# Kernel optimization log

Hardware: AMD Instinct MI355X
Metric: run time of the kernel (lower is better)

## Reference

```python
import jax, jax.numpy as jnp
import numpy as np

B, F, P, DM = 1, 16, 256, 1024            # batch, frames, patches, mm_hidden_size
HID = 4096                                 # config.hidden_size
DI, DSTATE, DTRANK, DCONV = 2 * DM, 16, DM // 16, 4


def _layernorm(x, w, b):
    mu = x.mean(-1, keepdims=True)
    var = ((x - mu) ** 2).mean(-1, keepdims=True)
    return (x - mu) * jax.lax.rsqrt(var + 1e-5) * w + b


def _selective_scan(u, dt, A, Bm, Cm, Dv):
    # u, dt: [b,L,d]; Bm, Cm: [b,L,n]; A: [d,n]; Dv: [d]
    def step(h, inp):
        dt_t, B_t, C_t, u_t = inp  # [b,d],[b,n],[b,n],[b,d]
        h = jnp.exp(dt_t[..., None] * A) * h + (dt_t * u_t)[..., None] * B_t[:, None, :]
        return h, jnp.einsum('bdn,bn->bd', h, C_t)
    h0 = jnp.zeros((u.shape[0], A.shape[0], A.shape[1]), u.dtype)
    _, ys = jax.lax.scan(step, h0, (jnp.swapaxes(dt, 0, 1), jnp.swapaxes(Bm, 0, 1),
                                    jnp.swapaxes(Cm, 0, 1), jnp.swapaxes(u, 0, 1)))
    return jnp.swapaxes(ys, 0, 1) + u * Dv


def _mamba_block(x, ln_w, ln_b, in_proj_w, conv_w, conv_b, x_proj_w,
                 dt_proj_w, dt_proj_b, A_log, D_param, out_proj_w):
    res = x
    x = _layernorm(x, ln_w, ln_b)
    xz = x @ in_proj_w                       # [b,L,2*DI]
    xin, z = jnp.split(xz, 2, axis=-1)
    xt = jnp.swapaxes(xin, 1, 2)             # [b,DI,L]
    xt = jax.lax.conv_general_dilated(xt, conv_w[:, None, :], (1,), [(DCONV - 1, 0)],
                                      dimension_numbers=('NCH', 'OIH', 'NCH'),
                                      feature_group_count=DI)
    xt = xt + conv_b[:, None]
    u = jax.nn.silu(jnp.swapaxes(xt, 1, 2))  # [b,L,DI]
    x_dbl = u @ x_proj_w                     # [b,L,DTRANK+2*DSTATE]
    dt_raw, Bm, Cm = jnp.split(x_dbl, [DTRANK, DTRANK + DSTATE], axis=-1)
    dt = jax.nn.softplus(dt_raw @ dt_proj_w + dt_proj_b)
    A = -jnp.exp(A_log)
    y = _selective_scan(u, dt, A, Bm, Cm, D_param)
    y = y * jax.nn.silu(z)
    return res + y @ out_proj_w


def setup_inputs() -> dict:
    key = jax.random.key(0)
    ks = jax.random.split(key, 8)
    s = 0.02
    return {
        'vst': jax.random.normal(ks[0], (B, F, P, DM), jnp.float32),
        'ln_w': jnp.ones((DM,), jnp.float32), 'ln_b': jnp.zeros((DM,), jnp.float32),
        'in_proj_w': jax.random.normal(ks[1], (DM, 2 * DI), jnp.float32) * s,
        'conv_w': jax.random.normal(ks[2], (DI, DCONV), jnp.float32) * s,
        'conv_b': jnp.zeros((DI,), jnp.float32),
        'x_proj_w': jax.random.normal(ks[3], (DI, DTRANK + 2 * DSTATE), jnp.float32) * s,
        'dt_proj_w': jax.random.normal(ks[4], (DTRANK, DI), jnp.float32) * s,
        'dt_proj_b': jnp.full((DI,), -4.6, jnp.float32),  # softplus ~ 0.01
        'A_log': jnp.log(jnp.tile(jnp.arange(1, DSTATE + 1, dtype=jnp.float32), (DI, 1))),
        'D_param': jnp.ones((DI,), jnp.float32),
        'out_proj_w': jax.random.normal(ks[5], (DI, DM), jnp.float32) * s,
        'fln_w': jnp.ones((DM,), jnp.float32), 'fln_b': jnp.zeros((DM,), jnp.float32),
        'mlp_w1': jax.random.normal(ks[6], (DM, HID), jnp.float32) * s,
        'mlp_b1': jnp.zeros((HID,), jnp.float32),
        'mlp_w2': jax.random.normal(ks[7], (HID, HID), jnp.float32) * s,
        'mlp_b2': jnp.zeros((HID,), jnp.float32),
    }


def reference(vst, ln_w, ln_b, in_proj_w, conv_w, conv_b, x_proj_w, dt_proj_w,
              dt_proj_b, A_log, D_param, out_proj_w, fln_w, fln_b,
              mlp_w1, mlp_b1, mlp_w2, mlp_b2):
    b, f, p, d = vst.shape
    h = w = int(p ** 0.5)
    # the chain of rearranges in the source is a net reshape to b (f h w) d
    x = vst.reshape(b, f * h * w, d)
    x = _mamba_block(x, ln_w, ln_b, in_proj_w, conv_w, conv_b, x_proj_w,
                     dt_proj_w, dt_proj_b, A_log, D_param, out_proj_w)
    x = _layernorm(x, fln_w, fln_b)
    # AvgPool3d kernel=(1,4,4), stride=(1,4,4) over (f,h,w)
    x = x.reshape(b, f, h // 4, 4, w // 4, 4, d).mean(axis=(3, 5))
    x = x.reshape(b, f * (h // 4) * (w // 4), d)
    y = jax.nn.gelu(x @ mlp_w1 + mlp_b1, approximate=False)
    return y @ mlp_w2 + mlp_b2
```

## Files before the change

kernel.cpp:

```cpp
#include <hip/hip_runtime.h>
#include <hip/hip_bf16.h>
#include <math.h>

typedef __hip_bfloat16 bf16_t;
typedef __attribute__((ext_vector_type(8))) short short8;
typedef __attribute__((ext_vector_type(4))) float f32x4;

#define L_SEQ   4096
#define DMODEL  1024
#define DI      2048
#define NST     16
#define DTRANK  64
#define XDBL_N  96
#define HID     4096
#define CHUNK   32
#define NCHUNK  128
#define POOLED_ROWS 256

__device__ __forceinline__ void async_load16(const bf16_t* g, bf16_t* l) {
    __builtin_amdgcn_global_load_lds(
        (const __attribute__((address_space(1))) void*)g,
        (__attribute__((address_space(3))) void*)l,
        16, 0, 0);
}

__device__ __forceinline__ float bfbits2f(unsigned short b) {
    bf16_t h; *(unsigned short*)&h = b; return __bfloat162float(h);
}

__global__ __launch_bounds__(256)
void transpose_all_kernel(const float* __restrict__ j0, bf16_t* __restrict__ o0,
                          const float* __restrict__ j1, bf16_t* __restrict__ o1,
                          const float* __restrict__ j2, bf16_t* __restrict__ o2,
                          const float* __restrict__ j3, bf16_t* __restrict__ o3,
                          const float* __restrict__ j4, bf16_t* __restrict__ o4,
                          const float* __restrict__ j5, bf16_t* __restrict__ o5) {
    int b = blockIdx.x;
    const float* in; bf16_t* out; int K, N, Npad, local;
    if (b < 512)        { in = j0; out = o0; K = 1024; N = 4096; Npad = 4096; local = b; }
    else if (b < 544)   { in = j1; out = o1; K = 2048; N = 96;   Npad = 128;  local = b - 512; }
    else if (b < 576)   { in = j2; out = o2; K = 64;   N = 2048; Npad = 2048; local = b - 544; }
    else if (b < 832)   { in = j3; out = o3; K = 2048; N = 1024; Npad = 1024; local = b - 576; }
    else if (b < 1344)  { in = j4; out = o4; K = 1024; N = 4096; Npad = 4096; local = b - 832; }
    else                { in = j5; out = o5; K = 4096; N = 4096; Npad = 4096; local = b - 1344; }
    int nt = Npad >> 6;
    int k0 = (local / nt) << 7, n0 = (local % nt) << 6;

    __shared__ float t[64 * 129];
    int tid = threadIdx.x;
    int kkb = tid >> 4;
    int nq  = (tid & 15) * 4;
#pragma unroll
    for (int it = 0; it < 8; it++) {
        int kl = it * 16 + kkb;
        int gk = k0 + kl, gn = n0 + nq;
        float4 v = {0.f, 0.f, 0.f, 0.f};
        if (gk < K) {
            const float* src = in + (size_t)gk * N + gn;
            if (gn + 3 < N) v = *(const float4*)src;
            else {
                if (gn + 0 < N) v.x = src[0];
                if (gn + 1 < N) v.y = src[1];
                if (gn + 2 < N) v.z = src[2];
                if (gn + 3 < N) v.w = src[3];
            }
        }
        t[(nq + 0) * 129 + kl] = v.x;
        t[(nq + 1) * 129 + kl] = v.y;
        t[(nq + 2) * 129 + kl] = v.z;
        t[(nq + 3) * 129 + kl] = v.w;
    }
    __syncthreads();
#pragma unroll
    for (int it = 0; it < 4; it++) {
        int slot = it * 256 + tid;
        int nn = slot >> 4, kc = (slot & 15) * 8;
        if (k0 + kc >= K) continue;
        const float* r = &t[nn * 129 + kc];
        short8 o;
#pragma unroll
        for (int j = 0; j < 8; j++) {
            bf16_t h = __float2bfloat16(r[j]);
            o[j] = *(short*)&h;
        }
        *(short8*)(out + (size_t)(n0 + nn) * K + k0 + kc) = o;
    }
}

__global__ __launch_bounds__(256)
void ln_kernel(const float* __restrict__ x, const float* __restrict__ w,
               const float* __restrict__ b, bf16_t* __restrict__ out) {
    int row = blockIdx.x;
    int tid = threadIdx.x;
    const float* xr = x + (size_t)row * DMODEL;
    float v[4];
    float s = 0.f, ss = 0.f;
#pragma unroll
    for (int e = 0; e < 4; e++) {
        v[e] = xr[tid + e * 256];
        s += v[e];
        ss += v[e] * v[e];
    }
#pragma unroll
    for (int off = 32; off > 0; off >>= 1) {
        s  += __shfl_down(s, off);
        ss += __shfl_down(ss, off);
    }
    __shared__ float rs[4], rss[4];
    int wid = tid >> 6;
    if ((tid & 63) == 0) { rs[wid] = s; rss[wid] = ss; }
    __syncthreads();
    s  = rs[0] + rs[1] + rs[2] + rs[3];
    ss = rss[0] + rss[1] + rss[2] + rss[3];
    float mu  = s * (1.f / DMODEL);
    float var = ss * (1.f / DMODEL) - mu * mu;
    float inv = rsqrtf(var + 1e-5f);
#pragma unroll
    for (int e = 0; e < 4; e++) {
        int col = tid + e * 256;
        out[(size_t)row * DMODEL + col] =
            __float2bfloat16((v[e] - mu) * inv * w[col] + b[col]);
    }
}

__global__ __launch_bounds__(256)
void ln_pool2_kernel(const bf16_t* __restrict__ part, size_t pstride,
                     const float* __restrict__ res, const float* __restrict__ w,
                     const float* __restrict__ b, bf16_t* __restrict__ pooled) {
    int p = blockIdx.x;
    int tid = threadIdx.x;
    int f = p >> 4, i4 = (p >> 2) & 3, j4 = p & 3;
    __shared__ float rs[4], rss[4];
    float acc[4] = {0.f, 0.f, 0.f, 0.f};
    float wv[4], bv[4];
#pragma unroll
    for (int e = 0; e < 4; e++) { wv[e] = w[tid + e * 256]; bv[e] = b[tid + e * 256]; }
    for (int r16 = 0; r16 < 16; r16++) {
        int ii = r16 >> 2, jj = r16 & 3;
        int row = f * 256 + (i4 * 4 + ii) * 16 + j4 * 4 + jj;
        size_t ro = (size_t)row * DMODEL;
        float v[4];
        float s = 0.f, ss = 0.f;
#pragma unroll
        for (int e = 0; e < 4; e++) {
            int col = tid + e * 256;
            float x = res[ro + col]
                    + __bfloat162float(part[ro + col])
                    + __bfloat162float(part[pstride + ro + col]);
            v[e] = x;
            s += x;
            ss += x * x;
        }
#pragma unroll
        for (int off = 32; off > 0; off >>= 1) {
            s  += __shfl_down(s, off);
            ss += __shfl_down(ss, off);
        }
        int wid = tid >> 6;
        if ((tid & 63) == 0) { rs[wid] = s; rss[wid] = ss; }
        __syncthreads();
        s  = rs[0] + rs[1] + rs[2] + rs[3];
        ss = rss[0] + rss[1] + rss[2] + rss[3];
        float mu  = s * (1.f / DMODEL);
        float var = ss * (1.f / DMODEL) - mu * mu;
        float inv = rsqrtf(var + 1e-5f);
#pragma unroll
        for (int e = 0; e < 4; e++)
            acc[e] += (v[e] - mu) * inv * wv[e] + bv[e];
        __syncthreads();
    }
#pragma unroll
    for (int e = 0; e < 4; e++)
        pooled[(size_t)p * DMODEL + tid + e * 256] = __float2bfloat16(acc[e] * (1.f / 16.f));
}

template <int EPI>
__global__ __launch_bounds__(256, 2)
void mfma_gemm(const bf16_t* __restrict__ A, int lda,
               const bf16_t* __restrict__ Bt, int ldb,
               int K,
               float* __restrict__ Cf, bf16_t* __restrict__ Cb, int ldc,
               const float* __restrict__ bias, const float* __restrict__ res) {
    __shared__ bf16_t Asl[128 * 32];
    __shared__ bf16_t Bsl[128 * 32];
    const int tid = threadIdx.x;
    const int l = tid & 63, w = tid >> 6;
    const int m0 = blockIdx.y * 128, n0 = blockIdx.x * 128;
    const int wm = (w >> 1) * 64, wn = (w & 1) * 64;

    const int srow = tid >> 2;
    const int skc = (tid & 3) * 8;
    const bf16_t* Ag = A + (size_t)(m0 + srow) * lda + skc;
    const bf16_t* Bg = Bt + (size_t)(n0 + srow) * ldb + skc;
    bf16_t* As0 = Asl + (size_t)(w * 64) * 8;
    bf16_t* As1 = Asl + (size_t)(256 + w * 64) * 8;
    bf16_t* Bs0 = Bsl + (size_t)(w * 64) * 8;
    bf16_t* Bs1 = Bsl + (size_t)(256 + w * 64) * 8;

    f32x4 acc[4][4];
#pragma unroll
    for (int i = 0; i < 4; i++)
#pragma unroll
        for (int j = 0; j < 4; j++) acc[i][j] = (f32x4){0.f, 0.f, 0.f, 0.f};

    const short8* Asv = (const short8*)Asl;
    const short8* Bsv = (const short8*)Bsl;
    const int fr = l >> 4;
    const int fc = l & 15;

    for (int k0 = 0; k0 < K; k0 += 32) {
        __syncthreads();
        async_load16(Ag, As0);
        async_load16(Ag + (size_t)64 * lda, As1);
        async_load16(Bg, Bs0);
        async_load16(Bg + (size_t)64 * ldb, Bs1);
        Ag += 32; Bg += 32;
        __syncthreads();

        short8 a[4], b[4];
#pragma unroll
        for (int im = 0; im < 4; im++)
            a[im] = Asv[(wm + im * 16 + fc) * 4 + fr];
#pragma unroll
        for (int in = 0; in < 4; in++)
            b[in] = Bsv[(wn + in * 16 + fc) * 4 + fr];
#pragma unroll
        for (int im = 0; im < 4; im++)
#pragma unroll
            for (int in = 0; in < 4; in++)
                acc[im][in] = __builtin_amdgcn_mfma_f32_16x16x32_bf16(
                    a[im], b[in], acc[im][in], 0, 0, 0);
    }

#pragma unroll
    for (int im = 0; im < 4; im++) {
        int mbase = m0 + wm + im * 16 + fr * 4;
#pragma unroll
        for (int in = 0; in < 4; in++) {
            int n = n0 + wn + in * 16 + fc;
            float bv = (EPI == 1) ? bias[n] : 0.f;
#pragma unroll
            for (int v = 0; v < 4; v++) {
                float x = acc[im][in][v];
                size_t off = (size_t)(mbase + v) * ldc + n;
                if (EPI == 0) {
                    Cb[off] = __float2bfloat16(x);
                } else if (EPI == 1) {
                    x += bv;
                    x = (x > 20.f) ? x : log1pf(__expf(x));
                    Cb[off] = __float2bfloat16(x);
                }
            }
        }
    }
}

template <bool PBF16>
__global__ __launch_bounds__(256, 2)
void mfma_gemm_splitk(const bf16_t* __restrict__ A, int lda,
                      const bf16_t* __restrict__ Bt, int ldb,
                      int Kper, void* __restrict__ Cpart, int ldc,
                      size_t pstride) {
    __shared__ bf16_t Asl[128 * 32];
    __shared__ bf16_t Bsl[128 * 32];
    const int tid = threadIdx.x;
    const int l = tid & 63, w = tid >> 6;
    const int m0 = blockIdx.y * 128, n0 = blockIdx.x * 128;
    const int wm = (w >> 1) * 64, wn = (w & 1) * 64;
    const int kbase = blockIdx.z * Kper;

    const int srow = tid >> 2;
    const int skc = (tid & 3) * 8;
    const bf16_t* Ag = A + (size_t)(m0 + srow) * lda + kbase + skc;
    const bf16_t* Bg = Bt + (size_t)(n0 + srow) * ldb + kbase + skc;
    bf16_t* As0 = Asl + (size_t)(w * 64) * 8;
    bf16_t* As1 = Asl + (size_t)(256 + w * 64) * 8;
    bf16_t* Bs0 = Bsl + (size_t)(w * 64) * 8;
    bf16_t* Bs1 = Bsl + (size_t)(256 + w * 64) * 8;

    f32x4 acc[4][4];
#pragma unroll
    for (int i = 0; i < 4; i++)
#pragma unroll
        for (int j = 0; j < 4; j++) acc[i][j] = (f32x4){0.f, 0.f, 0.f, 0.f};

    const short8* Asv = (const short8*)Asl;
    const short8* Bsv = (const short8*)Bsl;
    const int fr = l >> 4;
    const int fc = l & 15;

    for (int k0 = 0; k0 < Kper; k0 += 32) {
        __syncthreads();
        async_load16(Ag, As0);
        async_load16(Ag + (size_t)64 * lda, As1);
        async_load16(Bg, Bs0);
        async_load16(Bg + (size_t)64 * ldb, Bs1);
        Ag += 32; Bg += 32;
        __syncthreads();

        short8 a[4], b[4];
#pragma unroll
        for (int im = 0; im < 4; im++)
            a[im] = Asv[(wm + im * 16 + fc) * 4 + fr];
#pragma unroll
        for (int in = 0; in < 4; in++)
            b[in] = Bsv[(wn + in * 16 + fc) * 4 + fr];
#pragma unroll
        for (int im = 0; im < 4; im++)
#pragma unroll
            for (int in = 0; in < 4; in++)
                acc[im][in] = __builtin_amdgcn_mfma_f32_16x16x32_bf16(
                    a[im], b[in], acc[im][in], 0, 0, 0);
    }

#pragma unroll
    for (int im = 0; im < 4; im++) {
        int mbase = m0 + wm + im * 16 + fr * 4;
#pragma unroll
        for (int in = 0; in < 4; in++) {
            int n = n0 + wn + in * 16 + fc;
#pragma unroll
            for (int v = 0; v < 4; v++) {
                size_t o = (size_t)(mbase + v) * ldc + n;
                if (PBF16)
                    ((bf16_t*)Cpart)[(size_t)blockIdx.z * pstride + o] =
                        __float2bfloat16(acc[im][in][v]);
                else
                    ((float*)Cpart)[(size_t)blockIdx.z * pstride + o] = acc[im][in][v];
            }
        }
    }
}

template <int S, int EPI>
__global__ __launch_bounds__(256)
void reduce_splitk(const float* __restrict__ part, size_t pstride, int ldp,
                   int M, int N, float* __restrict__ outf, bf16_t* __restrict__ outb,
                   int ldo, const float* __restrict__ bias) {
    int idx = blockIdx.x * 256 + threadIdx.x;
    if (idx >= M * N) return;
    int r = idx / N, c = idx - r * N;
    float s = 0.f;
#pragma unroll
    for (int z = 0; z < S; z++)
        s += part[(size_t)z * pstride + (size_t)r * ldp + c];
    size_t o = (size_t)r * ldo + c;
    if (EPI == 0) {
        outf[o] = s;
        outb[o] = __float2bfloat16(s);
    } else if (EPI == 1) {
        s += bias[c];
        s = 0.5f * s * (1.f + erff(s * 0.70710678118654752f));
        outb[o] = __float2bfloat16(s);
    } else {
        outf[o] = s + bias[c];
    }
}

__global__ __launch_bounds__(256)
void conv_silu_kernel(const bf16_t* __restrict__ xz, const float* __restrict__ cw,
                      const float* __restrict__ cb, bf16_t* __restrict__ u) {
    int idx = blockIdx.x * 256 + threadIdx.x;
    if (idx >= L_SEQ * DI) return;
    int ch = idx & (DI - 1);
    int l  = idx >> 11;
    float acc = cb[ch];
#pragma unroll
    for (int k = 0; k < 4; k++) {
        int ls = l - 3 + k;
        if (ls >= 0)
            acc += cw[ch * 4 + k] * __bfloat162float(xz[(size_t)ls * (2 * DI) + ch]);
    }
    u[idx] = __float2bfloat16(acc / (1.f + __expf(-acc)));
}

__global__ __launch_bounds__(256)
void scan_pass1(const bf16_t* __restrict__ dt, const bf16_t* __restrict__ u,
                const float* __restrict__ x_dbl, const float* __restrict__ A_log,
                float* __restrict__ Pw, float* __restrict__ Sw) {
    int c = blockIdx.x;
    int tid = threadIdx.x;
    int lane = tid & 63, w = tid >> 6;
    int dloc = w * 32 + (lane & 31);
    int n0 = (lane >> 5) * 8;
    int d = blockIdx.y * 128 + dloc;
    int l0 = c * CHUNK;
    __shared__ float sB[CHUNK * NST];
    for (int i = tid; i < CHUNK * NST; i += 256)
        sB[i] = x_dbl[(size_t)(l0 + (i >> 4)) * XDBL_N + DTRANK + (i & 15)];
    __syncthreads();
    float Areg[8], h[8];
#pragma unroll
    for (int j = 0; j < 8; j++) {
        Areg[j] = -__expf(A_log[d * NST + n0 + j]);
        h[j] = 0.f;
    }
    float dts = 0.f;
    float dtl = __bfloat162float(dt[(size_t)l0 * DI + d]);
    float ul  = __bfloat162float(u[(size_t)l0 * DI + d]);
    for (int l = 0; l < CHUNK; l++) {
        float dtn = 0.f, un = 0.f;
        if (l + 1 < CHUNK) {
            int gl = l0 + l + 1;
            dtn = __bfloat162float(dt[(size_t)gl * DI + d]);
            un  = __bfloat162float(u[(size_t)gl * DI + d]);
        }
        float du = dtl * ul;
        dts += dtl;
#pragma unroll
        for (int j = 0; j < 8; j++) {
            float a = __expf(dtl * Areg[j]);
            h[j] = a * h[j] + du * sB[l * NST + n0 + j];
        }
        dtl = dtn; ul = un;
    }
    size_t base = ((size_t)c * DI + d) * NST + n0;
#pragma unroll
    for (int j = 0; j < 8; j++) {
        Pw[base + j] = __expf(dts * Areg[j]);
        Sw[base + j] = h[j];
    }
}

__global__ __launch_bounds__(256)
void scan_pass2(const float* __restrict__ Pw, float* __restrict__ SwInit) {
    int tid = blockIdx.x * 256 + threadIdx.x;
    if (tid >= DI * NST) return;
    const int DN = DI * NST;
    size_t idx = tid;
    float h = 0.f;
    float p = Pw[idx], s = SwInit[idx];
    for (int c = 0; c < NCHUNK; c++) {
        size_t nidx = idx + DN;
        float pn = 0.f, sn = 0.f;
        if (c + 1 < NCHUNK) { pn = Pw[nidx]; sn = SwInit[nidx]; }
        SwInit[idx] = h;
        h = p * h + s;
        p = pn; s = sn; idx = nidx;
    }
}

__global__ __launch_bounds__(256)
void scan_pass3(const bf16_t* __restrict__ dt, const bf16_t* __restrict__ u,
                const float* __restrict__ x_dbl, const float* __restrict__ A_log,
                const float* __restrict__ Dp, const float* __restrict__ initw,
                const bf16_t* __restrict__ xz, bf16_t* __restrict__ yy) {
    int c = blockIdx.x;
    int tid = threadIdx.x;
    int lane = tid & 63, w = tid >> 6;
    int dloc = w * 32 + (lane & 31);
    int n0 = (lane >> 5) * 8;
    int d = blockIdx.y * 128 + dloc;
    int l0 = c * CHUNK;
    __shared__ float sBC[CHUNK * 2 * NST];
    for (int i = tid; i < CHUNK * 2 * NST; i += 256)
        sBC[i] = x_dbl[(size_t)(l0 + (i >> 5)) * XDBL_N + DTRANK + (i & 31)];
    __syncthreads();
    float Areg[8], h[8];
    size_t base = ((size_t)c * DI + d) * NST + n0;
#pragma unroll
    for (int j = 0; j < 8; j++) {
        Areg[j] = -__expf(A_log[d * NST + n0 + j]);
        h[j] = initw[base + j];
    }
    float Dd = Dp[d];
    float dtl = __bfloat162float(dt[(size_t)l0 * DI + d]);
    float ul  = __bfloat162float(u[(size_t)l0 * DI + d]);
    float zv  = __bfloat162float(xz[(size_t)l0 * (2 * DI) + DI + d]);
    for (int l = 0; l < CHUNK; l++) {
        float dtn = 0.f, un = 0.f, zn = 0.f;
        if (l + 1 < CHUNK) {
            int gl = l0 + l + 1;
            dtn = __bfloat162float(dt[(size_t)gl * DI + d]);
            un  = __bfloat162float(u[(size_t)gl * DI + d]);
            zn  = __bfloat162float(xz[(size_t)gl * (2 * DI) + DI + d]);
        }
        float du = dtl * ul;
        float y = 0.f;
#pragma unroll
        for (int j = 0; j < 8; j++) {
            float a = __expf(dtl * Areg[j]);
            h[j] = a * h[j] + du * sBC[l * 32 + n0 + j];
            y += h[j] * sBC[l * 32 + NST + n0 + j];
        }
        y += __shfl_xor(y, 32);
        float sz = zv / (1.f + __expf(-zv));
        if ((lane >> 5) == 0)
            yy[(size_t)(l0 + l) * DI + d] = __float2bfloat16((y + ul * Dd) * sz);
        dtl = dtn; ul = un; zv = zn;
    }
}

extern "C" void kernel_launch(void* const* d_in, const int* in_sizes, int n_in,
                              void* d_out, int out_size, void* d_ws, size_t ws_size,
                              hipStream_t stream) {
    const float* vst        = (const float*)d_in[0];
    const float* ln_w       = (const float*)d_in[1];
    const float* ln_b       = (const float*)d_in[2];
    const float* in_proj_w  = (const float*)d_in[3];
    const float* conv_w     = (const float*)d_in[4];
    const float* conv_b     = (const float*)d_in[5];
    const float* x_proj_w   = (const float*)d_in[6];
    const float* dt_proj_w  = (const float*)d_in[7];
    const float* dt_proj_b  = (const float*)d_in[8];
    const float* A_log      = (const float*)d_in[9];
    const float* D_param    = (const float*)d_in[10];
    const float* out_proj_w = (const float*)d_in[11];
    const float* fln_w      = (const float*)d_in[12];
    const float* fln_b      = (const float*)d_in[13];
    const float* mlp_w1     = (const float*)d_in[14];
    const float* mlp_b1     = (const float*)d_in[15];
    const float* mlp_w2     = (const float*)d_in[16];
    const float* mlp_b2     = (const float*)d_in[17];
    float* out = (float*)d_out;

    char* wsb = (char*)d_ws;
    size_t off = 0;
    auto alloc_bf = [&](size_t n) { bf16_t* p = (bf16_t*)(wsb + off); off += n * 2; return p; };
    auto alloc_f  = [&](size_t n) { float*  p = (float*)(wsb + off); off += n * 4; return p; };

    bf16_t* w1t  = alloc_bf((size_t)(2 * DI) * DMODEL);
    bf16_t* xpt  = alloc_bf((size_t)128 * DI);
    bf16_t* dtpt = alloc_bf((size_t)DI * DTRANK);
    bf16_t* opt  = alloc_bf((size_t)DMODEL * DI);
    bf16_t* m1t  = alloc_bf((size_t)HID * DMODEL);
    bf16_t* m2t  = alloc_bf((size_t)HID * HID);
    bf16_t* xz_bf   = alloc_bf((size_t)L_SEQ * 2 * DI);
    bf16_t* u_bf    = alloc_bf((size_t)L_SEQ * DI);
    bf16_t* dt_bf   = alloc_bf((size_t)L_SEQ * DI);
    bf16_t* xdbl_bf = alloc_bf((size_t)L_SEQ * XDBL_N);
    bf16_t* yy_bf   = alloc_bf((size_t)L_SEQ * DI);
    float*  xdbl_f  = alloc_f((size_t)L_SEQ * XDBL_N);
    float*  Pw      = alloc_f((size_t)NCHUNK * DI * NST);
    float*  Sw      = alloc_f((size_t)NCHUNK * DI * NST);
    bf16_t* xn_bf   = yy_bf;
    float*  g2part  = Pw;
    bf16_t* g4part  = xz_bf;
    bf16_t* pooled  = dt_bf;
    bf16_t* h1_bf   = dt_bf + (size_t)POOLED_ROWS * DMODEL;
    float*  g5part  = (float*)yy_bf;
    float*  g6part  = (float*)xz_bf;

    dim3 blk256(256);

    transpose_all_kernel<<<3392, blk256, 0, stream>>>(
        in_proj_w, w1t, x_proj_w, xpt, dt_proj_w, dtpt,
        out_proj_w, opt, mlp_w1, m1t, mlp_w2, m2t);

    ln_kernel<<<L_SEQ, blk256, 0, stream>>>(vst, ln_w, ln_b, xn_bf);

    mfma_gemm<0><<<dim3((2 * DI) / 128, L_SEQ / 128), blk256, 0, stream>>>(
        xn_bf, DMODEL, w1t, DMODEL, DMODEL, nullptr, xz_bf, 2 * DI, nullptr, nullptr);

    conv_silu_kernel<<<(L_SEQ * DI) / 256, blk256, 0, stream>>>(xz_bf, conv_w, conv_b, u_bf);

    mfma_gemm_splitk<false><<<dim3(1, L_SEQ / 128, 8), blk256, 0, stream>>>(
        u_bf, DI, xpt, DI, DI / 8, g2part, 128, (size_t)L_SEQ * 128);
    reduce_splitk<8, 0><<<(L_SEQ * XDBL_N) / 256, blk256, 0, stream>>>(
        g2part, (size_t)L_SEQ * 128, 128, L_SEQ, XDBL_N, xdbl_f, xdbl_bf, XDBL_N, nullptr);

    mfma_gemm<1><<<dim3(DI / 128, L_SEQ / 128), blk256, 0, stream>>>(
        xdbl_bf, XDBL_N, dtpt, DTRANK, DTRANK, nullptr, dt_bf, DI, dt_proj_b, nullptr);

    scan_pass1<<<dim3(NCHUNK, DI / 128), blk256, 0, stream>>>(
        dt_bf, u_bf, xdbl_f, A_log, Pw, Sw);
    scan_pass2<<<(DI * NST) / 256, blk256, 0, stream>>>(Pw, Sw);
    scan_pass3<<<dim3(NCHUNK, DI / 128), blk256, 0, stream>>>(
        dt_bf, u_bf, xdbl_f, A_log, D_param, Sw, xz_bf, yy_bf);

    mfma_gemm_splitk<true><<<dim3(DMODEL / 128, L_SEQ / 128, 2), blk256, 0, stream>>>(
        yy_bf, DI, opt, DI, DI / 2, g4part, DMODEL, (size_t)L_SEQ * DMODEL);

    ln_pool2_kernel<<<POOLED_ROWS, blk256, 0, stream>>>(
        g4part, (size_t)L_SEQ * DMODEL, vst, fln_w, fln_b, pooled);

    mfma_gemm_splitk<false><<<dim3(HID / 128, POOLED_ROWS / 128, 4), blk256, 0, stream>>>(
        pooled, DMODEL, m1t, DMODEL, DMODEL / 4, g5part, HID, (size_t)POOLED_ROWS * HID);
    reduce_splitk<4, 1><<<(POOLED_ROWS * HID) / 256, blk256, 0, stream>>>(
        g5part, (size_t)POOLED_ROWS * HID, HID, POOLED_ROWS, HID, nullptr, h1_bf, HID, mlp_b1);

    mfma_gemm_splitk<false><<<dim3(HID / 128, POOLED_ROWS / 128, 8), blk256, 0, stream>>>(
        h1_bf, HID, m2t, HID, HID / 8, g6part, HID, (size_t)POOLED_ROWS * HID);
    reduce_splitk<8, 2><<<(POOLED_ROWS * HID) / 256, blk256, 0, stream>>>(
        g6part, (size_t)POOLED_ROWS * HID, HID, POOLED_ROWS, HID, out, nullptr, HID, mlp_b2);
}
```

Baseline: 483.6 us.

## Consume fp32 mlp_w2 directly in a new split-K GEMM, skipping its transpose

Stops transposing and converting the 4096x4096 mlp_w2 matrix to bf16 in the preprocessing kernel. A new 512-thread split-K MFMA kernel loads the fp32 weight tiles into LDS asynchronously and converts them to bf16 while building the fragments. This removes a full read and write pass over the largest weight matrix. In exchange, the final GEMM reads fp32 weights, twice the bytes of bf16, and does per-element conversions in its inner loop.

```diff
diff --git a/kernel.cpp b/kernel.cpp
--- a/kernel.cpp
+++ b/kernel.cpp
@@ -17,32 +17,26 @@
 #define NCHUNK  128
 #define POOLED_ROWS 256
 
-__device__ __forceinline__ void async_load16(const bf16_t* g, bf16_t* l) {
+__device__ __forceinline__ void async_load16(const void* g, void* l) {
     __builtin_amdgcn_global_load_lds(
         (const __attribute__((address_space(1))) void*)g,
         (__attribute__((address_space(3))) void*)l,
         16, 0, 0);
 }
 
-__device__ __forceinline__ float bfbits2f(unsigned short b) {
-    bf16_t h; *(unsigned short*)&h = b; return __bfloat162float(h);
-}
-
 __global__ __launch_bounds__(256)
 void transpose_all_kernel(const float* __restrict__ j0, bf16_t* __restrict__ o0,
                           const float* __restrict__ j1, bf16_t* __restrict__ o1,
                           const float* __restrict__ j2, bf16_t* __restrict__ o2,
                           const float* __restrict__ j3, bf16_t* __restrict__ o3,
-                          const float* __restrict__ j4, bf16_t* __restrict__ o4,
-                          const float* __restrict__ j5, bf16_t* __restrict__ o5) {
+                          const float* __restrict__ j4, bf16_t* __restrict__ o4) {
     int b = blockIdx.x;
     const float* in; bf16_t* out; int K, N, Npad, local;
     if (b < 512)        { in = j0; out = o0; K = 1024; N = 4096; Npad = 4096; local = b; }
     else if (b < 544)   { in = j1; out = o1; K = 2048; N = 96;   Npad = 128;  local = b - 512; }
     else if (b < 576)   { in = j2; out = o2; K = 64;   N = 2048; Npad = 2048; local = b - 544; }
     else if (b < 832)   { in = j3; out = o3; K = 2048; N = 1024; Npad = 1024; local = b - 576; }
-    else if (b < 1344)  { in = j4; out = o4; K = 1024; N = 4096; Npad = 4096; local = b - 832; }
-    else                { in = j5; out = o5; K = 4096; N = 4096; Npad = 4096; local = b - 1344; }
+    else                { in = j4; out = o4; K = 1024; N = 4096; Npad = 4096; local = b - 832; }
     int nt = Npad >> 6;
     int k0 = (local / nt) << 7, n0 = (local % nt) << 6;
 
@@ -328,6 +322,81 @@
                 else
                     ((float*)Cpart)[(size_t)blockIdx.z * pstride + o] = acc[im][in][v];
             }
+        }
+    }
+}
+
+__global__ __launch_bounds__(512, 1)
+void gemm_nt_kernel(const bf16_t* __restrict__ A, int lda,
+                    const float* __restrict__ B, int ldb,
+                    int Kper, float* __restrict__ Cpart, int ldc,
+                    size_t pstride) {
+    __shared__ bf16_t Asl[256 * 32];
+    __shared__ float  Bsl[32 * 64];
+    const int tid = threadIdx.x;
+    const int l = tid & 63, w = tid >> 6;
+    const int n0 = blockIdx.x * 64;
+    const int kbase = blockIdx.z * Kper;
+    const int wm = w * 32;
+
+    const int a_row = tid >> 2, a_kc = (tid & 3) * 8;
+    const bf16_t* Ag = A + (size_t)a_row * lda + kbase + a_kc;
+    bf16_t* As0 = Asl + (size_t)(w * 64) * 8;
+    bf16_t* As1 = Asl + (size_t)(512 + w * 64) * 8;
+    const int b_row = tid >> 4, b_nc = (tid & 15) * 4;
+    const float* Bg = B + (size_t)(kbase + b_row) * ldb + n0 + b_nc;
+    float* Bs0 = Bsl + (size_t)(w * 64) * 4;
+
+    f32x4 acc[2][4];
+#pragma unroll
+    for (int i = 0; i < 2; i++)
+#pragma unroll
+        for (int j = 0; j < 4; j++) acc[i][j] = (f32x4){0.f, 0.f, 0.f, 0.f};
+
+    const short8* Asv = (const short8*)Asl;
+    const int fr = l >> 4, fc = l & 15;
+
+    for (int k0 = 0; k0 < Kper; k0 += 32) {
+        __syncthreads();
+        async_load16(Ag, As0);
+        async_load16(Ag + (size_t)128 * lda, As1);
+        async_load16(Bg, Bs0);
+        Ag += 32;
+        Bg += (size_t)32 * ldb;
+        __syncthreads();
+
+        short8 a[2], bfr[4];
+        a[0] = Asv[(wm + fc) * 4 + fr];
+        a[1] = Asv[(wm + 16 + fc) * 4 + fr];
+#pragma unroll
+        for (int j = 0; j < 4; j++) {
+            const float* bp = Bsl + (size_t)(fr * 8) * 64 + j * 16 + fc;
+            short8 t;
+#pragma unroll
+            for (int i = 0; i < 8; i++) {
+                bf16_t h = __float2bfloat16(bp[i * 64]);
+                t[i] = *(short*)&h;
+            }
+            bfr[j] = t;
+        }
+#pragma unroll
+        for (int im = 0; im < 2; im++)
+#pragma unroll
+            for (int j = 0; j < 4; j++)
+                acc[im][j] = __builtin_amdgcn_mfma_f32_16x16x32_bf16(
+                    a[im], bfr[j], acc[im][j], 0, 0, 0);
+    }
+
+    float* Cz = Cpart + (size_t)blockIdx.z * pstride;
+#pragma unroll
+    for (int im = 0; im < 2; im++) {
+        int mbase = wm + im * 16 + fr * 4;
+#pragma unroll
+        for (int j = 0; j < 4; j++) {
+            int n = n0 + j * 16 + fc;
+#pragma unroll
+            for (int v = 0; v < 4; v++)
+                Cz[(size_t)(mbase + v) * ldc + n] = acc[im][j][v];
         }
     }
 }
@@ -524,7 +593,6 @@
     bf16_t* dtpt = alloc_bf((size_t)DI * DTRANK);
     bf16_t* opt  = alloc_bf((size_t)DMODEL * DI);
     bf16_t* m1t  = alloc_bf((size_t)HID * DMODEL);
-    bf16_t* m2t  = alloc_bf((size_t)HID * HID);
     bf16_t* xz_bf   = alloc_bf((size_t)L_SEQ * 2 * DI);
     bf16_t* u_bf    = alloc_bf((size_t)L_SEQ * DI);
     bf16_t* dt_bf   = alloc_bf((size_t)L_SEQ * DI);
@@ -543,9 +611,9 @@
 
     dim3 blk256(256);
 
-    transpose_all_kernel<<<3392, blk256, 0, stream>>>(
+    transpose_all_kernel<<<1344, blk256, 0, stream>>>(
         in_proj_w, w1t, x_proj_w, xpt, dt_proj_w, dtpt,
-        out_proj_w, opt, mlp_w1, m1t, mlp_w2, m2t);
+        out_proj_w, opt, mlp_w1, m1t);
 
     ln_kernel<<<L_SEQ, blk256, 0, stream>>>(vst, ln_w, ln_b, xn_bf);
 
@@ -579,8 +647,8 @@
     reduce_splitk<4, 1><<<(POOLED_ROWS * HID) / 256, blk256, 0, stream>>>(
         g5part, (size_t)POOLED_ROWS * HID, HID, POOLED_ROWS, HID, nullptr, h1_bf, HID, mlp_b1);
 
-    mfma_gemm_splitk<false><<<dim3(HID / 128, POOLED_ROWS / 128, 8), blk256, 0, stream>>>(
-        h1_bf, HID, m2t, HID, HID / 8, g6part, HID, (size_t)POOLED_ROWS * HID);
+    gemm_nt_kernel<<<dim3(HID / 64, 1, 8), dim3(512), 0, stream>>>(
+        h1_bf, HID, mlp_w2, HID, HID / 8, g6part, HID, (size_t)POOLED_ROWS * HID);
     reduce_splitk<8, 2><<<(POOLED_ROWS * HID) / 256, blk256, 0, stream>>>(
         g6part, (size_t)POOLED_ROWS * HID, HID, POOLED_ROWS, HID, out, nullptr, HID, mlp_b2);
 }
```

New measurement: 540.2 us. +11.7%, slower.
